# Optimization experiments

Measured on AMD Instinct MI355X. Metric: run time of the kernel, lower is better.

Reference implementation:

```python
import jax, jax.numpy as jnp
import numpy as np

V, H, L, NH, MAXS = 32000, 1024, 6, 16, 2048
HD = H // NH
FF = 4 * H
EPS = 1e-5


def _ln(x, s, b):
    m = jnp.mean(x, axis=-1, keepdims=True)
    v = jnp.mean(jnp.square(x - m), axis=-1, keepdims=True)
    return (x - m) * jax.lax.rsqrt(v + EPS) * s + b


def setup_inputs() -> dict:
    key = jax.random.key(0)
    ks = jax.random.split(key, 12)
    s = 0.02
    inp = {
        "input_ids": jax.random.randint(ks[0], (2, 1024), 0, V, dtype=jnp.int64),
        "token_emb": jax.random.normal(ks[1], (V, H), jnp.float32) * s,
        "pos_emb": jax.random.normal(ks[2], (MAXS, H), jnp.float32) * s,
        "ln1_s": jnp.ones((L, H), jnp.float32),
        "ln1_b": jnp.zeros((L, H), jnp.float32),
        "qkv_w": jax.random.normal(ks[3], (L, H, 3 * H), jnp.float32) * s,
        "qkv_b": jnp.zeros((L, 3 * H), jnp.float32),
        "out_w": jax.random.normal(ks[4], (L, H, H), jnp.float32) * s,
        "out_b": jnp.zeros((L, H), jnp.float32),
        "ln2_s": jnp.ones((L, H), jnp.float32),
        "ln2_b": jnp.zeros((L, H), jnp.float32),
        "w1": jax.random.normal(ks[5], (L, H, FF), jnp.float32) * s,
        "b1": jnp.zeros((L, FF), jnp.float32),
        "w2": jax.random.normal(ks[6], (L, FF, H), jnp.float32) * s,
        "b2": jnp.zeros((L, H), jnp.float32),
        "lnf_s": jnp.ones((H,), jnp.float32),
        "lnf_b": jnp.zeros((H,), jnp.float32),
        "lm_w": jax.random.normal(ks[7], (H, V), jnp.float32) * s,
    }
    return inp


def reference(input_ids, token_emb, pos_emb, ln1_s, ln1_b, qkv_w, qkv_b,
              out_w, out_b, ln2_s, ln2_b, w1, b1, w2, b2, lnf_s, lnf_b, lm_w):
    B, S = input_ids.shape
    x = token_emb[input_ids] + pos_emb[:S][None]  # [B,S,H]; dropout = identity (eval)
    for i in range(L):
        # --- attention block ---
        h = _ln(x, ln1_s[i], ln1_b[i])
        qkv = h @ qkv_w[i] + qkv_b[i]                      # [B,S,3H]
        q, k, v = jnp.split(qkv, 3, axis=-1)
        q = q.reshape(B, S, NH, HD)
        k = k.reshape(B, S, NH, HD)
        v = v.reshape(B, S, NH, HD)
        scores = jnp.einsum('bqhd,bkhd->bhqk', q, k) / jnp.sqrt(jnp.float32(HD))
        attn = jax.nn.softmax(scores, axis=-1)             # non-causal, as in source
        o = jnp.einsum('bhqk,bkhd->bqhd', attn, v).reshape(B, S, H)
        x = x + o @ out_w[i] + out_b[i]
        # --- mlp block ---
        h = _ln(x, ln2_s[i], ln2_b[i])
        h = jax.nn.gelu(h @ w1[i] + b1[i], approximate=False)
        x = x + h @ w2[i] + b2[i]
    x = _ln(x, lnf_s, lnf_b)
    logits = x @ lm_w                                      # [B,S,V]
    return logits
```

## Files before the change

kernel.cpp:

```cpp
#include <hip/hip_runtime.h>
#include <hip/hip_bf16.h>
#include <cstdint>
#include <cstddef>

typedef __bf16 bf16;
typedef __attribute__((ext_vector_type(8))) __bf16 bf16x8;
typedef __attribute__((ext_vector_type(4))) __bf16 bf16x4;
typedef __attribute__((ext_vector_type(4))) float f32x4;

__device__ __forceinline__ f32x4 mfma16(bf16x8 a, bf16x8 b, f32x4 c) {
    return __builtin_amdgcn_mfma_f32_16x16x32_bf16(a, b, c, 0, 0, 0);
}

__device__ __forceinline__ void async_copy16(const void* g, void* l) {
    __builtin_amdgcn_global_load_lds((const __attribute__((address_space(1))) void*)g,
                                     (__attribute__((address_space(3))) void*)l,
                                     16, 0, 0);
}

template<int Ncnt> __device__ __forceinline__ void waitv();
template<> __device__ __forceinline__ void waitv<0>() { asm volatile("s_waitcnt vmcnt(0)" ::: "memory"); }
template<> __device__ __forceinline__ void waitv<2>() { asm volatile("s_waitcnt vmcnt(2)" ::: "memory"); }
template<> __device__ __forceinline__ void waitv<3>() { asm volatile("s_waitcnt vmcnt(3)" ::: "memory"); }
template<> __device__ __forceinline__ void waitv<4>() { asm volatile("s_waitcnt vmcnt(4)" ::: "memory"); }

__device__ __forceinline__ void wait_g(int n) {
    if (n == 2) waitv<2>();
    else if (n == 3) waitv<3>();
    else waitv<4>();
}

__global__ __launch_bounds__(256)
void embed_kernel(const int* __restrict__ ids, const float* __restrict__ te,
                  const float* __restrict__ pe, float* __restrict__ x)
{
    const int row = blockIdx.x;
    const int s = row & 1023;
    const int id = ids[row];
    const f32x4* a = (const f32x4*)(te + (size_t)id * 1024);
    const f32x4* b = (const f32x4*)(pe + (size_t)s * 1024);
    f32x4* o = (f32x4*)(x + (size_t)row * 1024);
    o[threadIdx.x] = a[threadIdx.x] + b[threadIdx.x];
}

__device__ __forceinline__ void ln_body(const float* __restrict__ x, const float* __restrict__ sc,
                                        const float* __restrict__ bi, bf16* __restrict__ out,
                                        int row, int t, float* red)
{
    const f32x4 v = ((const f32x4*)(x + (size_t)row * 1024))[t];
    float s = v[0] + v[1] + v[2] + v[3];
    float q = v[0]*v[0] + v[1]*v[1] + v[2]*v[2] + v[3]*v[3];
    #pragma unroll
    for (int o = 1; o < 64; o <<= 1) { s += __shfl_xor(s, o); q += __shfl_xor(q, o); }
    const int wv = t >> 6, lane = t & 63;
    if (lane == 0) { red[wv] = s; red[4 + wv] = q; }
    __syncthreads();
    s = red[0] + red[1] + red[2] + red[3];
    q = red[4] + red[5] + red[6] + red[7];
    const float mean = s * (1.f / 1024.f);
    const float var  = q * (1.f / 1024.f) - mean * mean;
    const float rstd = rsqrtf(var + 1e-5f);
    const f32x4 scv = ((const f32x4*)sc)[t];
    const f32x4 biv = ((const f32x4*)bi)[t];
    bf16x4 o4;
    #pragma unroll
    for (int j = 0; j < 4; j++) o4[j] = (bf16)((v[j] - mean) * rstd * scv[j] + biv[j]);
    *(bf16x4*)(out + (size_t)row * 1024 + t * 4) = o4;
}

__device__ __forceinline__ void wcvt_body(const float* __restrict__ W, bf16* __restrict__ BT,
                                          int K, int N, int bid, int tidx, float (*tile)[65])
{
    const int nx = N >> 6;
    const int n0 = (bid % nx) << 6, k0 = (bid / nx) << 6;
    const int tx = tidx & 15, ty = tidx >> 4;
    #pragma unroll
    for (int r = 0; r < 4; r++) {
        const f32x4 v = *(const f32x4*)&W[(size_t)(k0 + ty + r*16) * N + n0 + tx*4];
        tile[ty + r*16][tx*4 + 0] = v[0];
        tile[ty + r*16][tx*4 + 1] = v[1];
        tile[ty + r*16][tx*4 + 2] = v[2];
        tile[ty + r*16][tx*4 + 3] = v[3];
    }
    __syncthreads();
    #pragma unroll
    for (int r = 0; r < 4; r++) {
        const int n = ty + r*16;
        bf16x4 o;
        #pragma unroll
        for (int j = 0; j < 4; j++) o[j] = (bf16)tile[tx*4 + j][n];
        *(bf16x4*)&BT[(size_t)(n0 + n) * K + k0 + tx*4] = o;
    }
}

__global__ __launch_bounds__(256)
void front_kernel(const float* __restrict__ x, const float* __restrict__ sc,
                  const float* __restrict__ bi, bf16* __restrict__ out,
                  const float* __restrict__ qkvw0, bf16* __restrict__ wTq,
                  const float* __restrict__ lmw, bf16* __restrict__ wTlm,
                  const float* __restrict__ outw, bf16* __restrict__ wTo_all)
{
    __shared__ float tile[64][65];
    __shared__ float red[8];
    const int bid = blockIdx.x, t = threadIdx.x;
    if (bid < 2048) {
        ln_body(x, sc, bi, out, bid, t, red);
    } else if (bid < 2048 + 768) {
        wcvt_body(qkvw0, wTq, 1024, 3072, bid - 2048, t, tile);
    } else if (bid < 2048 + 768 + 8000) {
        wcvt_body(lmw, wTlm, 1024, 32000, bid - 2816, t, tile);
    } else {
        const int wb = bid - 10816;
        const int l = wb >> 8;
        wcvt_body(outw + (size_t)l * 1024 * 1024, wTo_all + (size_t)l * 1024 * 1024,
                  1024, 1024, wb & 255, t, tile);
    }
}

__global__ __launch_bounds__(256)
void fused_ln_wcvt(const float* __restrict__ x, const float* __restrict__ sc,
                   const float* __restrict__ bi, bf16* __restrict__ out,
                   const float* __restrict__ W1, bf16* __restrict__ BT1, int K1, int N1, int nb1,
                   const float* __restrict__ W2, bf16* __restrict__ BT2, int K2, int N2)
{
    __shared__ float tile[64][65];
    __shared__ float red[8];
    const int bid = blockIdx.x, t = threadIdx.x;
    if (bid < 2048) {
        ln_body(x, sc, bi, out, bid, t, red);
    } else {
        const int wb = bid - 2048;
        if (wb < nb1) wcvt_body(W1, BT1, K1, N1, wb, t, tile);
        else          wcvt_body(W2, BT2, K2, N2, wb - nb1, t, tile);
    }
}

__global__ __launch_bounds__(256)
void attn_kernel(const bf16* __restrict__ qkv, const bf16* __restrict__ vT,
                 bf16* __restrict__ attno)
{
    __shared__ __align__(16) bf16 Ksh[128 * 64];
    __shared__ __align__(16) bf16 Vt[64 * 128];
    __shared__ __align__(16) bf16 Plds[4][16][132];

    const int bid = blockIdx.x, tid = threadIdx.x;
    const int b = (bid & 31) >> 4, h = bid & 15;
    const int qb = bid >> 5;
    const int lane = tid & 63, wave = tid >> 6;
    const bf16* base = qkv + (size_t)b * 1024 * 3072;
    const bf16* vbase = vT + (size_t)(b*16 + h) * 64 * 1024;
    const int qrow0 = qb * 64 + wave * 16;
    const int l15 = lane & 15;

    bf16x8 aQ[2];
    {
        const int qr = qrow0 + l15;
        const bf16* qp = base + (size_t)qr * 3072 + h * 64 + ((lane >> 4) << 3);
        aQ[0] = *(const bf16x8*)qp;
        aQ[1] = *(const bf16x8*)(qp + 32);
    }
    float m_i[4] = {-1e30f, -1e30f, -1e30f, -1e30f};
    float l_i[4] = {0.f, 0.f, 0.f, 0.f};
    f32x4 acc[4];
    #pragma unroll
    for (int nb = 0; nb < 4; nb++) acc[nb] = f32x4{0.f, 0.f, 0.f, 0.f};

    const int swzA = (((lane >> 4)     ^ (lane & 7)) << 3);
    const int swzB = (((4 + (lane >> 4)) ^ (lane & 7)) << 3);

    for (int ck = 0; ck < 8; ck++) {
        __syncthreads();
        #pragma unroll
        for (int p = 0; p < 4; p++) {
            const int c = p * 256 + tid;
            const int rw = c >> 3;
            const int kc = (c & 7) ^ (rw & 7);
            async_copy16(base + (size_t)(ck*128 + rw) * 3072 + 1024 + h*64 + kc*8, &Ksh[c * 8]);
        }
        #pragma unroll
        for (int p = 0; p < 4; p++) {
            const int c = p * 256 + tid;
            const int rw = c >> 4;
            const int kc = (c & 15) ^ (rw & 7);
            async_copy16(vbase + (size_t)rw * 1024 + ck*128 + kc*8, &Vt[c * 8]);
        }
        __syncthreads();

        f32x4 sc[8];
        #pragma unroll
        for (int kk = 0; kk < 4; kk++) {
            const int kr0 = (kk*32 + l15) * 64;
            const int kr1 = kr0 + 16*64;
            f32x4 z{0.f, 0.f, 0.f, 0.f};
            z = mfma16(aQ[0], *(const bf16x8*)&Ksh[kr0 + swzA], z);
            z = mfma16(aQ[1], *(const bf16x8*)&Ksh[kr0 + swzB], z);
            sc[2*kk] = z;
            f32x4 z2{0.f, 0.f, 0.f, 0.f};
            z2 = mfma16(aQ[0], *(const bf16x8*)&Ksh[kr1 + swzA], z2);
            z2 = mfma16(aQ[1], *(const bf16x8*)&Ksh[kr1 + swzB], z2);
            sc[2*kk+1] = z2;
        }

        float c[4];
        #pragma unroll
        for (int i = 0; i < 4; i++) {
            float t = sc[0][i];
            #pragma unroll
            for (int e = 1; e < 8; e++) t = fmaxf(t, sc[e][i]);
            #pragma unroll
            for (int o = 1; o < 16; o <<= 1) t = fmaxf(t, __shfl_xor(t, o));
            t *= 0.125f;
            const float mnew = fmaxf(m_i[i], t);
            c[i] = __expf(m_i[i] - mnew);
            float p[8];
            float rs = 0.f;
            #pragma unroll
            for (int e = 0; e < 8; e++) {
                p[e] = __expf(fmaf(sc[e][i], 0.125f, -mnew));
                rs += p[e];
            }
            #pragma unroll
            for (int o = 1; o < 16; o <<= 1) rs += __shfl_xor(rs, o);
            l_i[i] = l_i[i] * c[i] + rs;
            m_i[i] = mnew;
            const int pr = ((lane >> 4) << 2) + i;
            #pragma unroll
            for (int e = 0; e < 8; e++)
                Plds[wave][pr][(e >> 1) * 32 + (e & 1) * 16 + l15] = (bf16)p[e];
        }
        #pragma unroll
        for (int nb = 0; nb < 4; nb++) {
            f32x4 a = acc[nb];
            a[0] *= c[0]; a[1] *= c[1]; a[2] *= c[2]; a[3] *= c[3];
            acc[nb] = a;
        }

        #pragma unroll
        for (int kk = 0; kk < 4; kk++) {
            const bf16x8 aP = *(const bf16x8*)&Plds[wave][l15][kk*32 + ((lane >> 4) << 3)];
            #pragma unroll
            for (int nb = 0; nb < 4; nb++) {
                const int r = nb*16 + l15;
                const int chk = (kk*4 + (lane >> 4)) ^ (r & 7);
                const bf16x8 bV = *(const bf16x8*)&Vt[r*128 + chk*8];
                acc[nb] = mfma16(aP, bV, acc[nb]);
            }
        }
    }
    #pragma unroll
    for (int nb = 0; nb < 4; nb++) {
        #pragma unroll
        for (int i = 0; i < 4; i++) {
            const int row = qrow0 + ((lane >> 4) << 2) + i;
            const float o = acc[nb][i] / l_i[i];
            attno[(size_t)(b*1024 + row) * 1024 + h*64 + nb*16 + l15] = (bf16)o;
        }
    }
}

template<int BM, int BN, int EPI, int KSPLIT>
__global__ __launch_bounds__(512, 2)
void gemm256_kernel(const bf16* __restrict__ A, const bf16* __restrict__ BT,
                    const float* __restrict__ bias, float* __restrict__ resid,
                    bf16* __restrict__ outb, float* __restrict__ outf,
                    bf16* __restrict__ vt, int N, int K)
{
    constexpr int MT = 2048 / BM;
    constexpr int FM = BM / 32;
    constexpr int FN = BN / 64;
    constexpr int HM = FM / 2;
    constexpr int ACH = BM * 4;
    constexpr int BCH = BN * 4;
    constexpr int LA = (ACH + 511) >> 9;
    constexpr int LB = (BCH + 511) >> 9;
    constexpr int ASUB = BM * 32;
    constexpr int BSUB = BN * 32;
    extern __shared__ __align__(16) char smem_raw[];
    bf16* smem = (bf16*)smem_raw;

    const int nwg = gridDim.x;
    const int q = nwg >> 3, rr = nwg & 7;
    const int xcd = blockIdx.x & 7, ix = blockIdx.x >> 3;
    const int nid = (xcd < rr ? xcd * (q + 1) : rr * (q + 1) + (xcd - rr) * q) + ix;
    const int tiles = nwg / KSPLIT;
    const int ks = nid / tiles;
    const int tile = nid % tiles;
    const int bm = tile % MT, bn = tile / MT;

    const int tid = threadIdx.x, lane = tid & 63, wave = tid >> 6;
    const int wr = wave >> 2, wc = wave & 3;

    const int myB = ((BCH & 511) == 0) ? (BCH >> 9)
                    : ((tid < (BCH & 511)) ? (BCH >> 9) + 1 : (BCH >> 9));
    const int wcount = LA + myB;

    f32x4 acc[FM][FN];
    #pragma unroll
    for (int m = 0; m < FM; m++)
        #pragma unroll
        for (int n = 0; n < FN; n++) acc[m][n] = f32x4{0.f, 0.f, 0.f, 0.f};

    const bf16* Abase = A  + (size_t)bm * BM * K;
    const bf16* Bbase = BT + (size_t)bn * BN * K;
    const int Ts = (K >> 6) / KSPLIT;
    const int t0 = ks * Ts;

    const int l15 = lane & 15;
    const int swz = (((lane >> 4) ^ ((l15 >> 1) & 3)) << 3);
    const int arow0 = wr * (BM / 2) + l15;
    const int brow0 = wc * (BN / 4) + l15;

#define ABASE_(p_, ks_) (((p_)*2 + (ks_)) * ASUB)
#define BBASE_(p_, ks_) (4*ASUB + ((p_)*2 + (ks_)) * BSUB)
#define STAGE_A(p_, kt_, ks_) { _Pragma("unroll") for (int i = 0; i < LA; i++) { \
    const int c = tid + i * 512; \
    if ((ACH & 511) == 0 || c < ACH) { \
      const int rw = c >> 2; \
      const int kc = (c & 3) ^ ((rw >> 1) & 3); \
      async_copy16(Abase + (size_t)rw * K + (kt_)*64 + (ks_)*32 + kc*8, \
                   &smem[ABASE_(p_, ks_) + c*8]); } } }
#define STAGE_B(p_, kt_, ks_) { _Pragma("unroll") for (int i = 0; i < LB; i++) { \
    const int c = tid + i * 512; \
    if ((BCH & 511) == 0 || c < BCH) { \
      const int rw = c >> 2; \
      const int kc = (c & 3) ^ ((rw >> 1) & 3); \
      async_copy16(Bbase + (size_t)rw * K + (kt_)*64 + (ks_)*32 + kc*8, \
                   &smem[BBASE_(p_, ks_) + c*8]); } } }
#define LOAD_B(p_, ks_) { _Pragma("unroll") for (int n = 0; n < FN; n++) \
    bfv[n] = *(const bf16x8*)&smem[BBASE_(p_, ks_) + (brow0 + n*16)*32 + swz]; }
#define LOAD_A(p_, ks_, mg) { _Pragma("unroll") for (int m = 0; m < HM; m++) \
    af[m] = *(const bf16x8*)&smem[ABASE_(p_, ks_) + (arow0 + ((mg)*HM + m)*16)*32 + swz]; }
#define QUAD(mg) { __builtin_amdgcn_s_setprio(1); \
    _Pragma("unroll") for (int m = 0; m < HM; m++) \
      _Pragma("unroll") for (int n = 0; n < FN; n++) \
        acc[(mg)*HM + m][n] = mfma16(af[m], bfv[n], acc[(mg)*HM + m][n]); \
    __builtin_amdgcn_s_setprio(0); }

    STAGE_A(0, t0, 0); STAGE_B(0, t0, 0); STAGE_A(0, t0, 1); STAGE_B(0, t0, 1);
    wait_g(wcount);
    __builtin_amdgcn_s_barrier();

    for (int tl = 0; tl < Ts; tl++) {
        const int b = tl & 1;
        const int kt1 = t0 + tl + 1;
        const bool more = (tl + 1) < Ts;
        bf16x8 af[HM], bfv[FN];
        LOAD_B(b, 0); LOAD_A(b, 0, 0);
        if (more) STAGE_A(b ^ 1, kt1, 0);
        __builtin_amdgcn_s_barrier();
        QUAD(0);
        __builtin_amdgcn_s_barrier();
        LOAD_A(b, 0, 1);
        if (more) STAGE_B(b ^ 1, kt1, 0);
        __builtin_amdgcn_s_barrier();
        QUAD(1);
        if (more) wait_g(wcount); else waitv<0>();
        __builtin_amdgcn_s_barrier();
        LOAD_B(b, 1); LOAD_A(b, 1, 0);
        if (more) STAGE_A(b ^ 1, kt1, 1);
        __builtin_amdgcn_s_barrier();
        QUAD(0);
        __builtin_amdgcn_s_barrier();
        LOAD_A(b, 1, 1);
        if (more) STAGE_B(b ^ 1, kt1, 1);
        __builtin_amdgcn_s_barrier();
        QUAD(1);
        if (more) wait_g(wcount);
        __builtin_amdgcn_s_barrier();
    }

    const int er = bm * BM + wr * (BM / 2) + ((lane >> 4) << 2);
    const int ec = bn * BN + wc * (BN / 4) + l15;
    #pragma unroll
    for (int n = 0; n < FN; n++) {
        const int col = ec + n * 16;
        const float bv = (EPI == 3) ? 0.f : ((KSPLIT > 1 && ks != 0) ? 0.f : bias[col]);
        #pragma unroll
        for (int m = 0; m < FM; m++) {
            const int row0 = er + m * 16;
            if constexpr (EPI == 4) {
                if (col < 2048) {
                    #pragma unroll
                    for (int i = 0; i < 4; i++)
                        outb[(size_t)(row0 + i) * N + col] = (bf16)(acc[m][n][i] + bv);
                } else {
                    bf16x4 o4;
                    #pragma unroll
                    for (int i = 0; i < 4; i++) o4[i] = (bf16)(acc[m][n][i] + bv);
                    const int b_ = row0 >> 10, tok = row0 & 1023;
                    *(bf16x4*)&vt[((size_t)(b_ * 1024 + (col - 2048))) * 1024 + tok] = o4;
                }
            } else {
                #pragma unroll
                for (int i = 0; i < 4; i++) {
                    const float v = acc[m][n][i] + bv;
                    const size_t off = (size_t)(row0 + i) * N + col;
                    if constexpr (EPI == 0) outb[off] = (bf16)v;
                    else if constexpr (EPI == 1) {
                        if constexpr (KSPLIT > 1) atomicAdd(&resid[off], v);
                        else resid[off] += v;
                    }
                    else if constexpr (EPI == 2) {
                        outb[off] = (bf16)(0.5f * v * (1.f + erff(v * 0.70710678118f)));
                    } else {
                        outf[off] = v;
                    }
                }
            }
        }
    }
#undef ABASE_
#undef BBASE_
#undef STAGE_A
#undef STAGE_B
#undef LOAD_A
#undef LOAD_B
#undef QUAD
}

extern "C" void kernel_launch(void* const* d_in, const int* in_sizes, int n_in,
                              void* d_out, int out_size, void* d_ws, size_t ws_size,
                              hipStream_t stream)
{
    const int*   ids     = (const int*)  d_in[0];
    const float* tok_emb = (const float*)d_in[1];
    const float* pos_emb = (const float*)d_in[2];
    const float* ln1_s   = (const float*)d_in[3];
    const float* ln1_b   = (const float*)d_in[4];
    const float* qkv_w   = (const float*)d_in[5];
    const float* qkv_b   = (const float*)d_in[6];
    const float* out_w   = (const float*)d_in[7];
    const float* out_b   = (const float*)d_in[8];
    const float* ln2_s   = (const float*)d_in[9];
    const float* ln2_b   = (const float*)d_in[10];
    const float* w1      = (const float*)d_in[11];
    const float* b1      = (const float*)d_in[12];
    const float* w2      = (const float*)d_in[13];
    const float* b2      = (const float*)d_in[14];
    const float* lnf_s   = (const float*)d_in[15];
    const float* lnf_b   = (const float*)d_in[16];
    const float* lm_w    = (const float*)d_in[17];

    char* ws = (char*)d_ws;
    float* x    = (float*)ws;  ws += (size_t)2048 * 1024 * 4;
    bf16*  h    = (bf16*)ws;   ws += (size_t)2048 * 1024 * 2;
    bf16*  qkvb = (bf16*)ws;   ws += (size_t)2048 * 3072 * 2;
    bf16*  attno= (bf16*)ws;   ws += (size_t)2048 * 1024 * 2;
    bf16*  vT   = (bf16*)ws;   ws += (size_t)32 * 64 * 1024 * 2;
    bf16*  ff   = (bf16*)ws;   ws += (size_t)2048 * 4096 * 2;
    bf16*  wTq  = (bf16*)ws;   ws += (size_t)3072 * 1024 * 2;
    bf16*  wTo_all = (bf16*)ws; ws += (size_t)6 * 1024 * 1024 * 2;
    bf16*  wT1  = (bf16*)ws;   ws += (size_t)4096 * 1024 * 2;
    bf16*  wT2  = (bf16*)ws;   ws += (size_t)1024 * 4096 * 2;
    bf16*  wTlm = (bf16*)ws;   ws += (size_t)32000 * 1024 * 2;

    embed_kernel<<<2048, 256, 0, stream>>>(ids, tok_emb, pos_emb, x);

    for (int l = 0; l < 6; l++) {
        if (l == 0) {
            front_kernel<<<12352, 256, 0, stream>>>(
                x, ln1_s, ln1_b, h,
                qkv_w, wTq, lm_w, wTlm, out_w, wTo_all);
        } else {
            fused_ln_wcvt<<<2048 + 768, 256, 0, stream>>>(
                x, ln1_s + l*1024, ln1_b + l*1024, h,
                qkv_w + (size_t)l*1024*3072, wTq, 1024, 3072, 768,
                nullptr, nullptr, 0, 0);
        }
        gemm256_kernel<128,192,4,1><<<256, 512, 81920, stream>>>(
            h, wTq, qkv_b + l*3072, nullptr, qkvb, nullptr, vT, 3072, 1024);
        attn_kernel<<<512, 256, 0, stream>>>(qkvb, vT, attno);
        gemm256_kernel<128,256,1,4><<<256, 512, 98304, stream>>>(
            attno, wTo_all + (size_t)l*1024*1024, out_b + l*1024, x, nullptr, nullptr, nullptr, 1024, 1024);
        fused_ln_wcvt<<<2048 + 1024 + 1024, 256, 0, stream>>>(
            x, ln2_s + l*1024, ln2_b + l*1024, h,
            w1 + (size_t)l*1024*4096, wT1, 1024, 4096, 1024,
            w2 + (size_t)l*4096*1024, wT2, 4096, 1024);
        gemm256_kernel<128,256,2,1><<<256, 512, 98304, stream>>>(
            h, wT1, b1 + l*4096, nullptr, ff, nullptr, nullptr, 4096, 1024);
        gemm256_kernel<128,256,1,4><<<256, 512, 98304, stream>>>(
            ff, wT2, b2 + l*1024, x, nullptr, nullptr, nullptr, 1024, 4096);
    }
    fused_ln_wcvt<<<2048, 256, 0, stream>>>(
        x, lnf_s, lnf_b, h,
        nullptr, nullptr, 0, 0, 0,
        nullptr, nullptr, 0, 0);
    gemm256_kernel<256,256,3,1><<<8*125, 512, 131072, stream>>>(
        h, wTlm, nullptr, nullptr, nullptr, (float*)d_out, nullptr, 32000, 1024);
}
```

Baseline: 1.304 ms.

## Fuse embedding into front kernel, split attention barriers, add persistent LM-head GEMM

Folds the embedding gather into the first LayerNorm blocks of front_kernel, which removes one launch and one read of x. In the attention loop, the single K/V __syncthreads is replaced by a partial vmcnt wait, so K is waited on before QK and V only before PV. The LM-head GEMM now runs in a new persistent kernel: 256 workgroups with an XCD-aware tile order step through 1000 256x256 tiles, prefetch the next tile's first K slices while storing results with nontemporal stores, and use setprio around the MFMA groups. The risks are the hand-set vmcnt counts (4, 55), which must match how many loads are actually outstanding, and the extra register pressure from the larger tile.

```diff
diff --git a/kernel.cpp b/kernel.cpp
--- a/kernel.cpp
+++ b/kernel.cpp
@@ -23,6 +23,7 @@
 template<> __device__ __forceinline__ void waitv<2>() { asm volatile("s_waitcnt vmcnt(2)" ::: "memory"); }
 template<> __device__ __forceinline__ void waitv<3>() { asm volatile("s_waitcnt vmcnt(3)" ::: "memory"); }
 template<> __device__ __forceinline__ void waitv<4>() { asm volatile("s_waitcnt vmcnt(4)" ::: "memory"); }
+template<> __device__ __forceinline__ void waitv<55>() { asm volatile("s_waitcnt vmcnt(55)" ::: "memory"); }
 
 __device__ __forceinline__ void wait_g(int n) {
     if (n == 2) waitv<2>();
@@ -30,24 +31,10 @@
     else waitv<4>();
 }
 
-__global__ __launch_bounds__(256)
-void embed_kernel(const int* __restrict__ ids, const float* __restrict__ te,
-                  const float* __restrict__ pe, float* __restrict__ x)
-{
-    const int row = blockIdx.x;
-    const int s = row & 1023;
-    const int id = ids[row];
-    const f32x4* a = (const f32x4*)(te + (size_t)id * 1024);
-    const f32x4* b = (const f32x4*)(pe + (size_t)s * 1024);
-    f32x4* o = (f32x4*)(x + (size_t)row * 1024);
-    o[threadIdx.x] = a[threadIdx.x] + b[threadIdx.x];
-}
-
-__device__ __forceinline__ void ln_body(const float* __restrict__ x, const float* __restrict__ sc,
-                                        const float* __restrict__ bi, bf16* __restrict__ out,
-                                        int row, int t, float* red)
-{
-    const f32x4 v = ((const f32x4*)(x + (size_t)row * 1024))[t];
+__device__ __forceinline__ void ln_vec(f32x4 v, const float* __restrict__ sc,
+                                       const float* __restrict__ bi, bf16* __restrict__ out,
+                                       int row, int t, float* red)
+{
     float s = v[0] + v[1] + v[2] + v[3];
     float q = v[0]*v[0] + v[1]*v[1] + v[2]*v[2] + v[3]*v[3];
     #pragma unroll
@@ -68,6 +55,14 @@
     *(bf16x4*)(out + (size_t)row * 1024 + t * 4) = o4;
 }
 
+__device__ __forceinline__ void ln_body(const float* __restrict__ x, const float* __restrict__ sc,
+                                        const float* __restrict__ bi, bf16* __restrict__ out,
+                                        int row, int t, float* red)
+{
+    const f32x4 v = ((const f32x4*)(x + (size_t)row * 1024))[t];
+    ln_vec(v, sc, bi, out, row, t, red);
+}
+
 __device__ __forceinline__ void wcvt_body(const float* __restrict__ W, bf16* __restrict__ BT,
                                           int K, int N, int bid, int tidx, float (*tile)[65])
 {
@@ -94,8 +89,10 @@
 }
 
 __global__ __launch_bounds__(256)
-void front_kernel(const float* __restrict__ x, const float* __restrict__ sc,
-                  const float* __restrict__ bi, bf16* __restrict__ out,
+void front_kernel(const int* __restrict__ ids, const float* __restrict__ te,
+                  const float* __restrict__ pe, float* __restrict__ x,
+                  const float* __restrict__ sc, const float* __restrict__ bi,
+                  bf16* __restrict__ out,
                   const float* __restrict__ qkvw0, bf16* __restrict__ wTq,
                   const float* __restrict__ lmw, bf16* __restrict__ wTlm,
                   const float* __restrict__ outw, bf16* __restrict__ wTo_all)
@@ -104,7 +101,13 @@
     __shared__ float red[8];
     const int bid = blockIdx.x, t = threadIdx.x;
     if (bid < 2048) {
-        ln_body(x, sc, bi, out, bid, t, red);
+        const int s = bid & 1023;
+        const int id = ids[bid];
+        const f32x4 a = ((const f32x4*)(te + (size_t)id * 1024))[t];
+        const f32x4 b = ((const f32x4*)(pe + (size_t)s * 1024))[t];
+        const f32x4 v = a + b;
+        ((f32x4*)(x + (size_t)bid * 1024))[t] = v;
+        ln_vec(v, sc, bi, out, bid, t, red);
     } else if (bid < 2048 + 768) {
         wcvt_body(qkvw0, wTq, 1024, 3072, bid - 2048, t, tile);
     } else if (bid < 2048 + 768 + 8000) {
@@ -184,7 +187,9 @@
             const int kc = (c & 15) ^ (rw & 7);
             async_copy16(vbase + (size_t)rw * 1024 + ck*128 + kc*8, &Vt[c * 8]);
         }
-        __syncthreads();
+        waitv<4>();
+        __builtin_amdgcn_sched_barrier(0);
+        __builtin_amdgcn_s_barrier();
 
         f32x4 sc[8];
         #pragma unroll
@@ -228,13 +233,17 @@
             for (int e = 0; e < 8; e++)
                 Plds[wave][pr][(e >> 1) * 32 + (e & 1) * 16 + l15] = (bf16)p[e];
         }
+
+        waitv<0>();
+        __builtin_amdgcn_sched_barrier(0);
+        __builtin_amdgcn_s_barrier();
+
         #pragma unroll
         for (int nb = 0; nb < 4; nb++) {
             f32x4 a = acc[nb];
             a[0] *= c[0]; a[1] *= c[1]; a[2] *= c[2]; a[3] *= c[3];
             acc[nb] = a;
         }
-
         #pragma unroll
         for (int kk = 0; kk < 4; kk++) {
             const bf16x8 aP = *(const bf16x8*)&Plds[wave][l15][kk*32 + ((lane >> 4) << 3)];
@@ -418,6 +427,128 @@
 #undef QUAD
 }
 
+__global__ __launch_bounds__(512, 2)
+void gemm_lm_kernel(const bf16* __restrict__ A, const bf16* __restrict__ BT,
+                    float* __restrict__ outf, int N, int K, int NT)
+{
+    constexpr int ASUB = 256 * 32, BSUB = 256 * 32;
+    extern __shared__ __align__(16) char smem_raw[];
+    bf16* smem = (bf16*)smem_raw;
+
+    const int nwg = gridDim.x;
+    const int q = nwg >> 3, rr = nwg & 7;
+    const int xcd = blockIdx.x & 7, ix = blockIdx.x >> 3;
+    const int nid = (xcd < rr ? xcd * (q + 1) : rr * (q + 1) + (xcd - rr) * q) + ix;
+
+    const int tid = threadIdx.x, lane = tid & 63, wave = tid >> 6;
+    const int wr = wave >> 2, wc = wave & 3;
+    const int l15 = lane & 15;
+    const int swz = (((lane >> 4) ^ ((l15 >> 1) & 3)) << 3);
+    const int arow0 = wr * 128 + l15;
+    const int brow0 = wc * 64 + l15;
+    const int Ts = K >> 6;
+
+#define ABASE_(p_, ks_) (((p_)*2 + (ks_)) * ASUB)
+#define BBASE_(p_, ks_) (4*ASUB + ((p_)*2 + (ks_)) * BSUB)
+#define STG(base_, dst_, kt_, ks_) { _Pragma("unroll") for (int i = 0; i < 2; i++) { \
+    const int c = tid + i * 512; const int rw = c >> 2; \
+    const int kc = (c & 3) ^ ((rw >> 1) & 3); \
+    async_copy16((base_) + (size_t)rw * K + (kt_)*64 + (ks_)*32 + kc*8, \
+                 &smem[(dst_) + c*8]); } }
+#define LOAD_B(p_, ks_) { _Pragma("unroll") for (int n = 0; n < 4; n++) \
+    bfv[n] = *(const bf16x8*)&smem[BBASE_(p_, ks_) + (brow0 + n*16)*32 + swz]; }
+#define LOAD_A(p_, ks_, mg) { _Pragma("unroll") for (int m = 0; m < 4; m++) \
+    af[m] = *(const bf16x8*)&smem[ABASE_(p_, ks_) + (arow0 + ((mg)*4 + m)*16)*32 + swz]; }
+#define QUAD(mg) { __builtin_amdgcn_s_setprio(1); \
+    _Pragma("unroll") for (int m = 0; m < 4; m++) \
+      _Pragma("unroll") for (int n = 0; n < 4; n++) \
+        acc[(mg)*4 + m][n] = mfma16(af[m], bfv[n], acc[(mg)*4 + m][n]); \
+    __builtin_amdgcn_s_setprio(0); }
+
+    {
+        const int bm = nid & 7, bn = nid >> 3;
+        const bf16* Ab = A  + (size_t)bm * 256 * K;
+        const bf16* Bb = BT + (size_t)bn * 256 * K;
+        STG(Ab, ABASE_(0,0), 0, 0); STG(Bb, BBASE_(0,0), 0, 0);
+        STG(Ab, ABASE_(0,1), 0, 1); STG(Bb, BBASE_(0,1), 0, 1);
+        waitv<4>();
+        __builtin_amdgcn_s_barrier();
+    }
+
+    for (int ti = nid; ti < NT; ti += 256) {
+        const int bm = ti & 7, bn = ti >> 3;
+        const bf16* Abase = A  + (size_t)bm * 256 * K;
+        const bf16* Bbase = BT + (size_t)bn * 256 * K;
+        f32x4 acc[8][4];
+        #pragma unroll
+        for (int m = 0; m < 8; m++)
+            #pragma unroll
+            for (int n = 0; n < 4; n++) acc[m][n] = f32x4{0.f, 0.f, 0.f, 0.f};
+
+        for (int tl = 0; tl < Ts; tl++) {
+            const int b = tl & 1;
+            const int kt1 = tl + 1;
+            const bool more = (tl + 1) < Ts;
+            bf16x8 af[4], bfv[4];
+            LOAD_B(b, 0); LOAD_A(b, 0, 0);
+            if (more) STG(Abase, ABASE_(b ^ 1, 0), kt1, 0);
+            __builtin_amdgcn_s_barrier();
+            QUAD(0);
+            __builtin_amdgcn_s_barrier();
+            LOAD_A(b, 0, 1);
+            if (more) STG(Bbase, BBASE_(b ^ 1, 0), kt1, 0);
+            __builtin_amdgcn_s_barrier();
+            QUAD(1);
+            if (more) waitv<4>(); else waitv<0>();
+            __builtin_amdgcn_s_barrier();
+            LOAD_B(b, 1); LOAD_A(b, 1, 0);
+            if (more) STG(Abase, ABASE_(b ^ 1, 1), kt1, 1);
+            __builtin_amdgcn_s_barrier();
+            QUAD(0);
+            __builtin_amdgcn_s_barrier();
+            LOAD_A(b, 1, 1);
+            if (more) STG(Bbase, BBASE_(b ^ 1, 1), kt1, 1);
+            __builtin_amdgcn_s_barrier();
+            QUAD(1);
+            if (more) waitv<4>();
+            __builtin_amdgcn_s_barrier();
+        }
+
+        const bool has_next = (ti + 256) < NT;
+        if (has_next) {
+            const int nbm = (ti + 256) & 7, nbn = (ti + 256) >> 3;
+            const bf16* An = A  + (size_t)nbm * 256 * K;
+            const bf16* Bn = BT + (size_t)nbn * 256 * K;
+            STG(An, ABASE_(0,0), 0, 0); STG(Bn, BBASE_(0,0), 0, 0);
+            STG(An, ABASE_(0,1), 0, 1); STG(Bn, BBASE_(0,1), 0, 1);
+            __builtin_amdgcn_sched_barrier(0);
+        }
+        const int er = bm * 256 + wr * 128 + ((lane >> 4) << 2);
+        const int ec = bn * 256 + wc * 64 + l15;
+        #pragma unroll
+        for (int n = 0; n < 4; n++) {
+            const int col = ec + n * 16;
+            #pragma unroll
+            for (int m = 0; m < 8; m++) {
+                #pragma unroll
+                for (int i = 0; i < 4; i++)
+                    __builtin_nontemporal_store(acc[m][n][i],
+                        &outf[(size_t)(er + m * 16 + i) * N + col]);
+            }
+        }
+        if (has_next) {
+            waitv<55>();
+            __builtin_amdgcn_s_barrier();
+        }
+    }
+#undef ABASE_
+#undef BBASE_
+#undef STG
+#undef LOAD_A
+#undef LOAD_B
+#undef QUAD
+}
+
 extern "C" void kernel_launch(void* const* d_in, const int* in_sizes, int n_in,
                               void* d_out, int out_size, void* d_ws, size_t ws_size,
                               hipStream_t stream)
@@ -454,12 +585,10 @@
     bf16*  wT2  = (bf16*)ws;   ws += (size_t)1024 * 4096 * 2;
     bf16*  wTlm = (bf16*)ws;   ws += (size_t)32000 * 1024 * 2;
 
-    embed_kernel<<<2048, 256, 0, stream>>>(ids, tok_emb, pos_emb, x);
-
     for (int l = 0; l < 6; l++) {
         if (l == 0) {
             front_kernel<<<12352, 256, 0, stream>>>(
-                x, ln1_s, ln1_b, h,
+                ids, tok_emb, pos_emb, x, ln1_s, ln1_b, h,
                 qkv_w, wTq, lm_w, wTlm, out_w, wTo_all);
         } else {
             fused_ln_wcvt<<<2048 + 768, 256, 0, stream>>>(
@@ -485,6 +614,5 @@
         x, lnf_s, lnf_b, h,
         nullptr, nullptr, 0, 0, 0,
         nullptr, nullptr, 0, 0);
-    gemm256_kernel<256,256,3,1><<<8*125, 512, 131072, stream>>>(
-        h, wTlm, nullptr, nullptr, nullptr, (float*)d_out, nullptr, 32000, 1024);
-}
+    gemm_lm_kernel<<<256, 512, 131072, stream>>>(h, wTlm, (float*)d_out, 32000, 1024, 1000);
+}
```

Result: no change. 1.286 ms (-1.3%).
